# Optimization experiments

Measured on AMD Instinct MI355X. Metric: run time of the kernel, lower is better.

Reference implementation:

```python
import jax, jax.numpy as jnp
import numpy as np

B = 16        # graphs per batch
N0 = 4096     # nodes per graph (equal-size graphs -> static TopK shapes)
DEG = 8       # avg degree
E = B * N0 * DEG
CW = 64
OUT = 256


def _seg_sum(vals, idx, n):
    return jax.ops.segment_sum(vals, idx, num_segments=n)


def _sage(x, src, dst, valid, wl, bl, wr, n):
    # PyG SAGEConv: lin_l(mean_{j->i} x_j) + lin_r(x_i); lin_r has no bias
    vf = valid.astype(x.dtype)
    msg = x[src] * vf[:, None]                     # [E, d]
    s = _seg_sum(msg, dst, n)
    cnt = _seg_sum(vf, dst, n)
    mean = s / jnp.maximum(cnt, 1.0)[:, None]
    return mean @ wl.T + bl + x @ wr.T


def _gcn(x, src, dst, valid, w, b, n):
    # PyG GCNConv: add self-loops, symmetric normalization
    h = x @ w.T
    vf = valid.astype(x.dtype)
    deg = 1.0 + _seg_sum(vf, dst, n)               # includes self-loop
    inv_sqrt = jax.lax.rsqrt(deg)
    norm = inv_sqrt[src] * inv_sqrt[dst] * vf      # [E]
    agg = _seg_sum(h[src] * norm[:, None], dst, n) + h * (1.0 / deg)[:, None]
    return agg + b


def _topk_pool(x, src, dst, valid, w, n_per_graph):
    # PyG TopKPooling: score = x@w/||w||, keep top ceil(ratio*n) per graph,
    # x' = x[perm] * tanh(score[perm]); reindex edges, drop edges with removed endpoints.
    k = (n_per_graph + 1) // 2
    score = (x @ w) / jnp.linalg.norm(w)
    vals, idx = jax.lax.top_k(score.reshape(B, n_per_graph), k)   # [B,k]
    offs = (jnp.arange(B, dtype=jnp.int32) * n_per_graph)[:, None]
    perm = (idx.astype(jnp.int32) + offs).reshape(-1)             # [B*k] global ids
    x_new = x[perm] * jnp.tanh(vals.reshape(-1))[:, None]
    new_idx = jnp.full((B * n_per_graph,), -1, dtype=jnp.int32).at[perm].set(
        jnp.arange(B * k, dtype=jnp.int32))
    s2, d2 = new_idx[src], new_idx[dst]
    valid2 = valid & (s2 >= 0) & (d2 >= 0)
    s2 = jnp.where(valid2, s2, 0)
    d2 = jnp.where(valid2, d2, 0)
    return x_new, s2, d2, valid2, k


def _readout(x, k):
    xg = x.reshape(B, k, -1)
    return jnp.concatenate([xg.max(axis=1), xg.mean(axis=1)], axis=1)  # [B, 2d]


def _forward(x, edge_src, edge_dst, w1_l, b1, w1_r, w2_l, b2, w2_r, w3_l, b3, w3_r,
             w4, b4, w5, b5, w6, b6, p1, p2, p3, p4, p5, p6,
             lw1, lb1, lw2, lb2, lw3, lb3):
    src, dst = edge_src, edge_dst
    valid = jnp.ones((E,), dtype=bool)
    n = N0
    sage_ps = [(w1_l, b1, w1_r), (w2_l, b2, w2_r), (w3_l, b3, w3_r)]
    gcn_ps = [(w4, b4), (w5, b5), (w6, b6)]
    pools = [p1, p2, p3, p4, p5, p6]
    h = x
    z = None
    for i in range(6):
        if i < 3:
            wl, bl, wr = sage_ps[i]
            h = jax.nn.relu(_sage(h, src, dst, valid, wl, bl, wr, B * n))
        else:
            w, b = gcn_ps[i - 3]
            h = jax.nn.relu(_gcn(h, src, dst, valid, w, b, B * n))
        h, src, dst, valid, n = _topk_pool(h, src, dst, valid, pools[i], n)
        r = _readout(h, n)
        z = r if z is None else z + r
    z = jax.nn.relu(z @ lw1.T + lb1)
    z = jax.nn.relu(z @ lw2.T + lb2)
    z = z @ lw3.T + lb3
    return jax.nn.softmax(z, axis=1)


def setup_inputs() -> dict:
    key = jax.random.key(0)
    ks = jax.random.split(key, 40)

    def nrm(k, shape, s=0.1):
        return jax.random.normal(k, shape, dtype=jnp.float32) * s

    # per-graph random edges (both endpoints inside the same graph block)
    epg = N0 * DEG
    src_l = jax.random.randint(ks[0], (B, epg), 0, N0, dtype=jnp.int32)
    dst_l = jax.random.randint(ks[1], (B, epg), 0, N0, dtype=jnp.int32)
    offs = (jnp.arange(B, dtype=jnp.int32) * N0)[:, None]
    inp = {
        'x': jax.random.normal(ks[2], (B * N0, 2), dtype=jnp.float32),
        'edge_src': (src_l + offs).reshape(-1),
        'edge_dst': (dst_l + offs).reshape(-1),
        'w1_l': nrm(ks[3], (CW, 2)), 'b1': nrm(ks[4], (CW,)), 'w1_r': nrm(ks[5], (CW, 2)),
        'w2_l': nrm(ks[6], (CW, CW)), 'b2': nrm(ks[7], (CW,)), 'w2_r': nrm(ks[8], (CW, CW)),
        'w3_l': nrm(ks[9], (CW, CW)), 'b3': nrm(ks[10], (CW,)), 'w3_r': nrm(ks[11], (CW, CW)),
        'w4': nrm(ks[12], (CW, CW)), 'b4': jnp.zeros((CW,), jnp.float32),
        'w5': nrm(ks[13], (CW, CW)), 'b5': jnp.zeros((CW,), jnp.float32),
        'w6': nrm(ks[14], (CW, CW)), 'b6': jnp.zeros((CW,), jnp.float32),
        'p1': nrm(ks[15], (CW,)), 'p2': nrm(ks[16], (CW,)), 'p3': nrm(ks[17], (CW,)),
        'p4': nrm(ks[18], (CW,)), 'p5': nrm(ks[19], (CW,)), 'p6': nrm(ks[20], (CW,)),
        'lw1': nrm(ks[21], (128, 2 * CW)), 'lb1': nrm(ks[22], (128,)),
        'lw2': nrm(ks[23], (64, 128)), 'lb2': nrm(ks[24], (64,)),
        'lw3': nrm(ks[25], (OUT, 64)), 'lb3': nrm(ks[26], (OUT,)),
    }
    return inp


def reference(x, edge_src, edge_dst, w1_l, b1, w1_r, w2_l, b2, w2_r, w3_l, b3, w3_r,
              w4, b4, w5, b5, w6, b6, p1, p2, p3, p4, p5, p6,
              lw1, lb1, lw2, lb2, lw3, lb3):
    return _forward(x, edge_src, edge_dst, w1_l, b1, w1_r, w2_l, b2, w2_r,
                    w3_l, b3, w3_r, w4, b4, w5, b5, w6, b6,
                    p1, p2, p3, p4, p5, p6, lw1, lb1, lw2, lb2, lw3, lb3)
```

## Files before the change

kernel.cpp:

```cpp
#include <hip/hip_runtime.h>
#include <math.h>

#define NB 16
#define N0 4096
#define NE 524288


static __global__ void k_count(const int* __restrict__ dst, int* __restrict__ cnt) {
  int e = blockIdx.x * 256 + threadIdx.x;
  if (e >= NE) return;
  atomicAdd(&cnt[dst[e]], 1);
}

static __global__ void k_fill0(const int* __restrict__ src, const int* __restrict__ dst,
                               int* __restrict__ cursor, int* __restrict__ list) {
  int e = blockIdx.x * 256 + threadIdx.x;
  if (e >= NE) return;
  int d = dst[e];
  int slot = atomicAdd(&cursor[d], 1);
  list[slot] = src[e];
}


static __global__ void k_scan1(const int* __restrict__ in, int* __restrict__ out,
                               int* __restrict__ bsum, int n) {
  __shared__ int ts[256];
  int base = blockIdx.x * 1024 + threadIdx.x * 4;
  int a0 = (base + 0 < n) ? in[base + 0] : 0;
  int a1 = (base + 1 < n) ? in[base + 1] : 0;
  int a2 = (base + 2 < n) ? in[base + 2] : 0;
  int a3 = (base + 3 < n) ? in[base + 3] : 0;
  int s = a0 + a1 + a2 + a3;
  ts[threadIdx.x] = s;
  __syncthreads();
  for (int off = 1; off < 256; off <<= 1) {
    int v = (threadIdx.x >= off) ? ts[threadIdx.x - off] : 0;
    __syncthreads();
    ts[threadIdx.x] += v;
    __syncthreads();
  }
  int excl = ts[threadIdx.x] - s;
  if (base + 0 < n) out[base + 0] = excl;
  excl += a0;
  if (base + 1 < n) out[base + 1] = excl;
  excl += a1;
  if (base + 2 < n) out[base + 2] = excl;
  excl += a2;
  if (base + 3 < n) out[base + 3] = excl;
  if (threadIdx.x == 255) bsum[blockIdx.x] = ts[255];
}

static __global__ void k_scan2(int* __restrict__ bsum, int nb) {
  __shared__ int t[64];
  int i = threadIdx.x;
  int v = (i < nb) ? bsum[i] : 0;
  t[i] = v;
  __syncthreads();
  for (int off = 1; off < 64; off <<= 1) {
    int u = (i >= off) ? t[i - off] : 0;
    __syncthreads();
    t[i] += u;
    __syncthreads();
  }
  if (i < nb) bsum[i] = t[i] - v;
}

static __global__ void k_scan3(int* __restrict__ out, const int* __restrict__ bsum, int n) {
  int i = blockIdx.x * 256 + threadIdx.x;
  if (i < n) out[i] += bsum[i >> 10];
}


static __global__ void k_newcount(const int* __restrict__ perm, const int* __restrict__ offs,
                                  const int* __restrict__ cnt, const int* __restrict__ list,
                                  const int* __restrict__ newidx, int* __restrict__ ncnt,
                                  int newn) {
  int nn = blockIdx.x * 256 + threadIdx.x;
  if (nn >= newn) return;
  int old = perm[nn];
  int st = offs[old], c = cnt[old];
  int cc = 0;
  for (int j = 0; j < c; ++j) cc += (newidx[list[st + j]] >= 0);
  ncnt[nn] = cc;
}

static __global__ void k_newfill(const int* __restrict__ perm, const int* __restrict__ offs,
                                 const int* __restrict__ cnt, const int* __restrict__ list,
                                 const int* __restrict__ newidx, const int* __restrict__ noffs,
                                 int* __restrict__ nlist, int newn) {
  int nn = blockIdx.x * 256 + threadIdx.x;
  if (nn >= newn) return;
  int old = perm[nn];
  int st = offs[old], c = cnt[old];
  int pos = noffs[nn];
  for (int j = 0; j < c; ++j) {
    int s2 = newidx[list[st + j]];
    if (s2 >= 0) nlist[pos++] = s2;
  }
}


static __global__ void k_pnorm(const float* __restrict__ p0, const float* __restrict__ p1,
                               const float* __restrict__ p2, const float* __restrict__ p3,
                               const float* __restrict__ p4, const float* __restrict__ p5,
                               float* __restrict__ pnbuf) {
  const float* pp = p0;
  switch (blockIdx.x) {
    case 1: pp = p1; break;
    case 2: pp = p2; break;
    case 3: pp = p3; break;
    case 4: pp = p4; break;
    case 5: pp = p5; break;
    default: break;
  }
  double v = (double)pp[threadIdx.x];
  v *= v;
#pragma unroll
  for (int off = 1; off < 64; off <<= 1) v += __shfl_xor(v, off);
  if (threadIdx.x == 0) pnbuf[blockIdx.x] = (float)(1.0 / sqrt(v));
}


static __global__ void k_sage_gather2(const float* __restrict__ x, const int* __restrict__ offs,
                                      const int* __restrict__ cnt, const int* __restrict__ list,
                                      float* __restrict__ mean, int ntot) {
  int v = blockIdx.x * 256 + threadIdx.x;
  if (v >= ntot) return;
  int st = offs[v], c = cnt[v];
  float s0 = 0.f, s1 = 0.f;
  for (int j = 0; j < c; ++j) {
    int s = list[st + j];
    s0 += x[s * 2 + 0];
    s1 += x[s * 2 + 1];
  }
  float inv = 1.0f / fmaxf((float)c, 1.0f);
  mean[v * 2 + 0] = s0 * inv;
  mean[v * 2 + 1] = s1 * inv;
}

static __global__ void k_sage_gather64(const float* __restrict__ x, const int* __restrict__ offs,
                                       const int* __restrict__ cnt, const int* __restrict__ list,
                                       float* __restrict__ mean, int ntot) {
  int lane = threadIdx.x & 63, vl = threadIdx.x >> 6;
  int v = blockIdx.x * 4 + vl;
  if (v >= ntot) return;
  int st = offs[v], c = cnt[v];
  float acc = 0.f;
  for (int j = 0; j < c; ++j) {
    int s = list[st + j];
    acc += x[(size_t)s * 64 + lane];
  }
  mean[(size_t)v * 64 + lane] = acc * (1.0f / fmaxf((float)c, 1.0f));
}

static __global__ void k_sage0(const float* __restrict__ x, const float* __restrict__ mean,
                               const float* __restrict__ wl, const float* __restrict__ blv,
                               const float* __restrict__ wr, const float* __restrict__ pvec,
                               const float* __restrict__ pnbuf, float* __restrict__ h,
                               float* __restrict__ score, int ntot) {
  __shared__ float wlT[2][65], wrT[2][65];
  if (threadIdx.x < 128) {
    int o = threadIdx.x >> 1, d = threadIdx.x & 1;
    wlT[d][o] = wl[o * 2 + d];
    wrT[d][o] = wr[o * 2 + d];
  }
  __syncthreads();
  int o = threadIdx.x & 63, vl = threadIdx.x >> 6;
  int base = blockIdx.x * 16 + vl * 4;
  float pn = pnbuf[0];
  float psl = pvec[o];
#pragma unroll
  for (int r = 0; r < 4; ++r) {
    int v = base + r;
    if (v >= ntot) break;
    float acc = blv[o] + mean[v * 2 + 0] * wlT[0][o] + mean[v * 2 + 1] * wlT[1][o] +
                x[v * 2 + 0] * wrT[0][o] + x[v * 2 + 1] * wrT[1][o];
    float hval = fmaxf(acc, 0.0f);
    h[(size_t)v * 64 + o] = hval;
    double sc = (double)hval * (double)psl;
#pragma unroll
    for (int off = 1; off < 64; off <<= 1) sc += __shfl_xor(sc, off);
    if (o == 0) score[v] = (float)sc * pn;
  }
}

static __global__ __launch_bounds__(256) void k_sage_mm(
    const float* __restrict__ x, const float* __restrict__ mean, const float* __restrict__ wl,
    const float* __restrict__ blv, const float* __restrict__ wr, const float* __restrict__ pvec,
    const float* __restrict__ pnbuf, int pidx, float* __restrict__ h,
    float* __restrict__ score) {
  __shared__ float smem[16384];
  __shared__ float psh[64], bsh[64];
  float* xT = smem;
  float* mT = smem + 4096;
  float* wlT = smem + 8192;
  float* wrT = smem + 12288;
  int t = threadIdx.x;
  size_t nb = blockIdx.x;

  const float4* wl4 = (const float4*)wl;
  const float4* wr4 = (const float4*)wr;
  for (int i4 = t; i4 < 1024; i4 += 256) {
    int o = i4 >> 4, db = (i4 & 15) << 2;
    float4 L = wl4[i4], R = wr4[i4];
    float Lv[4] = {L.x, L.y, L.z, L.w}, Rv[4] = {R.x, R.y, R.z, R.w};
    int og = o >> 2, o3 = o & 3;
#pragma unroll
    for (int j = 0; j < 4; ++j) {
      int d = db + j;
      int col = ((og ^ (d & 15)) << 2) | o3;
      wlT[(d << 6) + col] = Lv[j];
      wrT[(d << 6) + col] = Rv[j];
    }
  }
  if (t < 64) {
    psh[t] = pvec[t];
    bsh[t] = blv[t];
  }
  const float4* x4 = (const float4*)(x + nb * 4096);
  const float4* m4 = (const float4*)(mean + nb * 4096);
  for (int i = t; i < 1024; i += 256) {
    int node = i >> 4, db = (i & 15) << 2;
    float4 a = x4[i], m = m4[i];
    float av[4] = {a.x, a.y, a.z, a.w}, mv[4] = {m.x, m.y, m.z, m.w};
    int ng = node >> 2, n0 = node & 3;
#pragma unroll
    for (int j = 0; j < 4; ++j) {
      int d = db + j;
      int col = ((ng ^ (d & 15)) << 2) | n0;
      xT[(d << 6) + col] = av[j];
      mT[(d << 6) + col] = mv[j];
    }
  }
  __syncthreads();

  int tx = t & 15, ty = t >> 4;
  float acc[4][4] = {};
#pragma unroll 4
  for (int k = 0; k < 64; ++k) {
    int s = k & 15;
    int ca = (tx ^ s) << 2, cb = (ty ^ s) << 2;
    const float4 a = *(const float4*)&xT[(k << 6) + ca];
    const float4 m = *(const float4*)&mT[(k << 6) + ca];
    const float4 L = *(const float4*)&wlT[(k << 6) + cb];
    const float4 R = *(const float4*)&wrT[(k << 6) + cb];
    float A[4] = {a.x, a.y, a.z, a.w}, M[4] = {m.x, m.y, m.z, m.w};
    float Lv[4] = {L.x, L.y, L.z, L.w}, Rv[4] = {R.x, R.y, R.z, R.w};
#pragma unroll
    for (int r = 0; r < 4; ++r)
#pragma unroll
      for (int c = 0; c < 4; ++c) acc[r][c] += M[r] * Lv[c] + A[r] * Rv[c];
  }

  float pn = pnbuf[pidx];
  float hv[4][4];
  double sp[4];
#pragma unroll
  for (int r = 0; r < 4; ++r) {
    sp[r] = 0.0;
#pragma unroll
    for (int c = 0; c < 4; ++c) {
      float v = fmaxf(acc[r][c] + bsh[(ty << 2) + c], 0.0f);
      hv[r][c] = v;
      sp[r] += (double)v * (double)psh[(ty << 2) + c];
    }
  }
  __syncthreads();
  float* hT = smem;
  double* sred = (double*)(smem + 8192);
#pragma unroll
  for (int r = 0; r < 4; ++r) {
    int node = (tx << 2) + r;
    int nk = node & 15;
#pragma unroll
    for (int c = 0; c < 4; ++c) hT[node * 68 + (((ty ^ nk) << 2) | c)] = hv[r][c];
    sred[(ty << 6) + node] = sp[r];
  }
  __syncthreads();
  float4* h4 = (float4*)(h + nb * 4096);
  for (int i = t; i < 1024; i += 256) {
    int node = i >> 4, q = i & 15;
    h4[i] = *(const float4*)&hT[node * 68 + ((q ^ (node & 15)) << 2)];
  }
  if (t < 64) {
    double ssum = 0.0;
    for (int g = 0; g < 16; ++g) ssum += sred[(g << 6) + t];
    score[nb * 64 + t] = (float)ssum * pn;
  }
}

static __global__ __launch_bounds__(256) void k_gcn_mm(const float* __restrict__ x,
                                                       const float* __restrict__ w,
                                                       float* __restrict__ h1) {
  __shared__ float smem[8192];
  float* xT = smem;
  float* wT = smem + 4096;
  int t = threadIdx.x;
  size_t nb = blockIdx.x;
  const float4* w4 = (const float4*)w;
  for (int i4 = t; i4 < 1024; i4 += 256) {
    int o = i4 >> 4, db = (i4 & 15) << 2;
    float4 W = w4[i4];
    float Wv[4] = {W.x, W.y, W.z, W.w};
    int og = o >> 2, o3 = o & 3;
#pragma unroll
    for (int j = 0; j < 4; ++j) {
      int d = db + j;
      wT[(d << 6) + (((og ^ (d & 15)) << 2) | o3)] = Wv[j];
    }
  }
  const float4* x4 = (const float4*)(x + nb * 4096);
  for (int i = t; i < 1024; i += 256) {
    int node = i >> 4, db = (i & 15) << 2;
    float4 a = x4[i];
    float av[4] = {a.x, a.y, a.z, a.w};
    int ng = node >> 2, n0 = node & 3;
#pragma unroll
    for (int j = 0; j < 4; ++j) {
      int d = db + j;
      xT[(d << 6) + (((ng ^ (d & 15)) << 2) | n0)] = av[j];
    }
  }
  __syncthreads();
  int tx = t & 15, ty = t >> 4;
  float acc[4][4] = {};
#pragma unroll 4
  for (int k = 0; k < 64; ++k) {
    int s = k & 15;
    const float4 a = *(const float4*)&xT[(k << 6) + ((tx ^ s) << 2)];
    const float4 W = *(const float4*)&wT[(k << 6) + ((ty ^ s) << 2)];
    float A[4] = {a.x, a.y, a.z, a.w}, Wv[4] = {W.x, W.y, W.z, W.w};
#pragma unroll
    for (int r = 0; r < 4; ++r)
#pragma unroll
      for (int c = 0; c < 4; ++c) acc[r][c] += A[r] * Wv[c];
  }
  __syncthreads();
  float* hT = smem;
#pragma unroll
  for (int r = 0; r < 4; ++r) {
    int node = (tx << 2) + r;
    int nk = node & 15;
#pragma unroll
    for (int c = 0; c < 4; ++c) hT[node * 68 + (((ty ^ nk) << 2) | c)] = acc[r][c];
  }
  __syncthreads();
  float4* h4 = (float4*)(h1 + nb * 4096);
  for (int i = t; i < 1024; i += 256) {
    int node = i >> 4, q = i & 15;
    h4[i] = *(const float4*)&hT[node * 68 + ((q ^ (node & 15)) << 2)];
  }
}

static __global__ void k_gcn_gather(const float* __restrict__ h1, const int* __restrict__ offs,
                                    const int* __restrict__ cnt, const int* __restrict__ list,
                                    const float* __restrict__ b, const float* __restrict__ pvec,
                                    const float* __restrict__ pnbuf, int pidx,
                                    float* __restrict__ h, float* __restrict__ score, int ntot) {
  int lane = threadIdx.x & 63, vl = threadIdx.x >> 6;
  int v = blockIdx.x * 4 + vl;
  if (v >= ntot) return;
  int st = offs[v], c = cnt[v];
  float degv = 1.0f + (float)c;
  float ivd = 1.0f / sqrtf(degv);
  float acc = 0.f;
  for (int j = 0; j < c; ++j) {
    int s = list[st + j];
    float nrm = (1.0f / sqrtf(1.0f + (float)cnt[s])) * ivd;
    acc += h1[(size_t)s * 64 + lane] * nrm;
  }
  float outv = fmaxf(acc + h1[(size_t)v * 64 + lane] * (1.0f / degv) + b[lane], 0.0f);
  h[(size_t)v * 64 + lane] = outv;
  double sc = (double)outv * (double)pvec[lane];
#pragma unroll
  for (int off = 1; off < 64; off <<= 1) sc += __shfl_xor(sc, off);
  if (lane == 0) score[v] = (float)sc * pnbuf[pidx];
}


static __global__ void k_chunksort(const float* __restrict__ score,
                                   unsigned long long* __restrict__ runs, int n_per, int k,
                                   int* __restrict__ newidx, int* __restrict__ perm, int single) {
  extern __shared__ unsigned long long sk[];
  int CH = blockDim.x;
  int g0 = blockIdx.x * CH;
  int b = g0 / n_per;
  int i = threadIdx.x;
  int gi = g0 + i;
  int li = gi - b * n_per;
  unsigned u = __float_as_uint(score[gi]);
  unsigned s = (u & 0x80000000u) ? u : ~(u | 0x80000000u);
  sk[i] = ((unsigned long long)s << 32) | (unsigned)li;
  __syncthreads();
  for (int ksz = 2; ksz <= CH; ksz <<= 1) {
    for (int j = ksz >> 1; j > 0; j >>= 1) {
      int ixj = i ^ j;
      if (ixj > i) {
        unsigned long long a = sk[i], c = sk[ixj];
        bool up = ((i & ksz) == 0);
        if ((a > c) == up) {
          sk[i] = c;
          sk[ixj] = a;
        }
      }
      __syncthreads();
    }
  }
  if (!single) {
    runs[gi] = sk[i];
  } else {
    int r = i;
    int idx = (int)(sk[r] & 0xFFFFFFFFu);
    int gidx = b * n_per + idx;
    if (r < k) {
      perm[b * k + r] = gidx;
      newidx[gidx] = b * k + r;
    } else {
      newidx[gidx] = -1;
    }
  }
}

static __global__ void k_merge(const unsigned long long* __restrict__ in,
                               unsigned long long* __restrict__ out, int L, int ntot, int n_per,
                               int k, int* __restrict__ newidx, int* __restrict__ perm,
                               int final) {
  int g = blockIdx.x * 256 + threadIdx.x;
  if (g >= ntot) return;
  unsigned long long key = in[g];
  int pair = g / (2 * L);
  int base = pair * 2 * L;
  int t = g - base;
  const unsigned long long* sib;
  int p;
  if (t < L) {
    sib = in + base + L;
    p = t;
  } else {
    sib = in + base;
    p = t - L;
  }
  int lo = 0, hi = L;
  while (lo < hi) {
    int mid = (lo + hi) >> 1;
    lo = (sib[mid] < key) ? mid + 1 : lo;
    hi = (sib[mid] < key) ? hi : mid;
  }
  int pos = p + lo;
  if (!final) {
    out[base + pos] = key;
  } else {
    int b = base / n_per;
    int idx = (int)(key & 0xFFFFFFFFu);
    int gidx = b * n_per + idx;
    if (pos < k) {
      perm[b * k + pos] = gidx;
      newidx[gidx] = b * k + pos;
    } else {
      newidx[gidx] = -1;
    }
  }
}

static __global__ void k_gather(const float* __restrict__ h, const float* __restrict__ score,
                                const int* __restrict__ perm, float* __restrict__ xnew, int kt) {
  int t = blockIdx.x * 256 + threadIdx.x;
  if (t >= kt * 16) return;
  int nn = t >> 4, q = t & 15;
  int old = perm[nn];
  float tm = tanhf(score[old]);
  float4 v = *(const float4*)&h[(size_t)old * 64 + q * 4];
  v.x *= tm; v.y *= tm; v.z *= tm; v.w *= tm;
  *(float4*)&xnew[(size_t)nn * 64 + q * 4] = v;
}


static __global__ void k_readout_part(const float* __restrict__ xnew, float* __restrict__ pmax,
                                      float* __restrict__ psum, int k, int nch) {
  int b = blockIdx.x / nch, c = blockIdx.x % nch;
  int d = threadIdx.x & 63, sl = threadIdx.x >> 6;
  int rpc = k / nch;
  const float* p = xnew + ((size_t)b * k + (size_t)c * rpc) * 64 + d;
  float m = -INFINITY, s = 0.0f;
  for (int r = sl; r < rpc; r += 4) {
    float v = p[(size_t)r * 64];
    m = fmaxf(m, v);
    s += v;
  }
  __shared__ float sm[4][64], ss[4][64];
  sm[sl][d] = m;
  ss[sl][d] = s;
  __syncthreads();
  if (sl == 0) {
    m = fmaxf(fmaxf(sm[0][d], sm[1][d]), fmaxf(sm[2][d], sm[3][d]));
    s = ss[0][d] + ss[1][d] + ss[2][d] + ss[3][d];
    pmax[(size_t)blockIdx.x * 64 + d] = m;
    psum[(size_t)blockIdx.x * 64 + d] = s;
  }
}

static __global__ void k_readout_comb(const float* __restrict__ pmax,
                                      const float* __restrict__ psum, float* __restrict__ z,
                                      int k, int nch) {
  int b = blockIdx.x, d = threadIdx.x;
  float m = -INFINITY, s = 0.0f;
  for (int c = 0; c < nch; ++c) {
    m = fmaxf(m, pmax[((size_t)b * nch + c) * 64 + d]);
    s += psum[((size_t)b * nch + c) * 64 + d];
  }
  z[b * 128 + d] += m;
  z[b * 128 + 64 + d] += s / (float)k;
}


static __global__ void k_mlp(const float* __restrict__ z, const float* __restrict__ lw1,
                             const float* __restrict__ lb1, const float* __restrict__ lw2,
                             const float* __restrict__ lb2, const float* __restrict__ lw3,
                             const float* __restrict__ lb3, float* __restrict__ out) {
  __shared__ float zs[128], t1[128], t2[64], t3[256], red[256];
  int b = blockIdx.x, tid = threadIdx.x;
  if (tid < 128) zs[tid] = z[b * 128 + tid];
  __syncthreads();
  if (tid < 128) {
    double a = 0.0;
    for (int d = 0; d < 128; ++d) a += (double)lw1[tid * 128 + d] * (double)zs[d];
    t1[tid] = fmaxf((float)a + lb1[tid], 0.0f);
  }
  __syncthreads();
  if (tid < 64) {
    double a = 0.0;
    for (int d = 0; d < 128; ++d) a += (double)lw2[tid * 128 + d] * (double)t1[d];
    t2[tid] = fmaxf((float)a + lb2[tid], 0.0f);
  }
  __syncthreads();
  {
    double a = 0.0;
    for (int d = 0; d < 64; ++d) a += (double)lw3[tid * 64 + d] * (double)t2[d];
    t3[tid] = (float)a + lb3[tid];
  }
  __syncthreads();
  red[tid] = t3[tid];
  __syncthreads();
  for (int s = 128; s > 0; s >>= 1) {
    if (tid < s) red[tid] = fmaxf(red[tid], red[tid + s]);
    __syncthreads();
  }
  float mx = red[0];
  __syncthreads();
  float e = expf(t3[tid] - mx);
  red[tid] = e;
  __syncthreads();
  for (int s = 128; s > 0; s >>= 1) {
    if (tid < s) red[tid] += red[tid + s];
    __syncthreads();
  }
  out[b * 256 + tid] = e / red[0];
}


extern "C" void kernel_launch(void* const* d_in, const int* in_sizes, int n_in,
                              void* d_out, int out_size, void* d_ws, size_t ws_size,
                              hipStream_t stream) {
  const float* x0 = (const float*)d_in[0];
  const int* esrc0 = (const int*)d_in[1];
  const int* edst0 = (const int*)d_in[2];
  const float* WL[3] = {(const float*)d_in[3], (const float*)d_in[6], (const float*)d_in[9]};
  const float* BL[3] = {(const float*)d_in[4], (const float*)d_in[7], (const float*)d_in[10]};
  const float* WR[3] = {(const float*)d_in[5], (const float*)d_in[8], (const float*)d_in[11]};
  const float* WG[3] = {(const float*)d_in[12], (const float*)d_in[14], (const float*)d_in[16]};
  const float* BG[3] = {(const float*)d_in[13], (const float*)d_in[15], (const float*)d_in[17]};
  const float* P[6] = {(const float*)d_in[18], (const float*)d_in[19], (const float*)d_in[20],
                       (const float*)d_in[21], (const float*)d_in[22], (const float*)d_in[23]};
  const float* lw1 = (const float*)d_in[24];
  const float* lb1 = (const float*)d_in[25];
  const float* lw2 = (const float*)d_in[26];
  const float* lb2 = (const float*)d_in[27];
  const float* lw3 = (const float*)d_in[28];
  const float* lb3 = (const float*)d_in[29];

  char* ws = (char*)d_ws;
  size_t off = 0;
  auto alloc = [&](size_t bytes) -> void* {
    void* p = ws + off;
    off += (bytes + 255) & ~(size_t)255;
    return p;
  };
  float* hA = (float*)alloc((size_t)65536 * 64 * 4);
  float* hB = (float*)alloc((size_t)32768 * 64 * 4);
  float* mean = (float*)alloc((size_t)32768 * 64 * 4);
  float* tmp = (float*)alloc((size_t)8192 * 64 * 4);
  float* score = (float*)alloc((size_t)65536 * 4);
  int* newidx = (int*)alloc((size_t)65536 * 4);
  int* perm = (int*)alloc((size_t)32768 * 4);
  int* cntA = (int*)alloc((size_t)65536 * 4);
  int* cntB = (int*)alloc((size_t)65536 * 4);
  int* offsA = (int*)alloc((size_t)65536 * 4);
  int* offsB = (int*)alloc((size_t)65536 * 4);
  int* cursor = (int*)alloc((size_t)65536 * 4);
  int* bsum = (int*)alloc((size_t)64 * 4);
  int* listA = (int*)alloc((size_t)NE * 4);
  int* listB = (int*)alloc((size_t)NE * 4);
  float* z = (float*)alloc((size_t)16 * 128 * 4);
  float* pmax = (float*)alloc((size_t)NB * 32 * 64 * 4);
  float* psum = (float*)alloc((size_t)NB * 32 * 64 * 4);
  unsigned long long* keyA = (unsigned long long*)alloc((size_t)65536 * 8);
  unsigned long long* keyB = (unsigned long long*)alloc((size_t)65536 * 8);
  float* pnbuf = (float*)alloc((size_t)64 * 4);
  if (off > ws_size) return;

  auto scan = [&](int* cntp, int* offsp, int n) {
    int nblk = (n + 1023) / 1024;
    k_scan1<<<nblk, 256, 0, stream>>>(cntp, offsp, bsum, n);
    k_scan2<<<1, 64, 0, stream>>>(bsum, nblk);
    k_scan3<<<(n + 255) / 256, 256, 0, stream>>>(offsp, bsum, n);
  };

  hipMemsetAsync(z, 0, 16 * 128 * 4, stream);
  k_pnorm<<<6, 64, 0, stream>>>(P[0], P[1], P[2], P[3], P[4], P[5], pnbuf);

  hipMemsetAsync(cntA, 0, (size_t)65536 * 4, stream);
  k_count<<<NE / 256, 256, 0, stream>>>(edst0, cntA);
  scan(cntA, offsA, 65536);
  hipMemcpyAsync(cursor, offsA, (size_t)65536 * 4, hipMemcpyDeviceToDevice, stream);
  k_fill0<<<NE / 256, 256, 0, stream>>>(esrc0, edst0, cursor, listA);

  const float* xcur = x0;
  int* ccnt = cntA;
  int* coffs = offsA;
  int* clist = listA;

  for (int i = 0; i < 6; ++i) {
    int n_per = N0 >> i;
    int ntot = NB * n_per;
    int k = n_per >> 1;

    if (i == 0) {
      k_sage_gather2<<<(ntot + 255) / 256, 256, 0, stream>>>(xcur, coffs, ccnt, clist, mean, ntot);
      k_sage0<<<(ntot + 15) / 16, 256, 0, stream>>>(xcur, mean, WL[0], BL[0], WR[0], P[0], pnbuf,
                                                    hA, score, ntot);
    } else if (i < 3) {
      k_sage_gather64<<<(ntot + 3) / 4, 256, 0, stream>>>(xcur, coffs, ccnt, clist, mean, ntot);
      k_sage_mm<<<ntot / 64, 256, 0, stream>>>(xcur, mean, WL[i], BL[i], WR[i], P[i], pnbuf, i,
                                               hA, score);
    } else {
      int g = i - 3;
      k_gcn_mm<<<ntot / 64, 256, 0, stream>>>(xcur, WG[g], tmp);
      k_gcn_gather<<<(ntot + 3) / 4, 256, 0, stream>>>(tmp, coffs, ccnt, clist, BG[g], P[i],
                                                       pnbuf, i, hA, score, ntot);
    }

    int CH = (n_per < 256) ? n_per : 256;
    int single = (CH == n_per) ? 1 : 0;
    k_chunksort<<<ntot / CH, CH, (size_t)CH * 8, stream>>>(score, keyA, n_per, k, newidx, perm,
                                                           single);
    if (!single) {
      unsigned long long* cur = keyA;
      unsigned long long* nxt = keyB;
      for (int L = CH; L * 2 <= n_per; L <<= 1) {
        int fin = (L * 2 == n_per) ? 1 : 0;
        k_merge<<<(ntot + 255) / 256, 256, 0, stream>>>(cur, nxt, L, ntot, n_per, k, newidx, perm,
                                                        fin);
        unsigned long long* t = cur;
        cur = nxt;
        nxt = t;
      }
    }
    k_gather<<<(NB * k * 16 + 255) / 256, 256, 0, stream>>>(hA, score, perm, hB, NB * k);

    if (i < 5) {
      int newn = NB * k;
      int* ncnt = (i & 1) ? cntA : cntB;
      int* noffs = (i & 1) ? offsA : offsB;
      int* nlist = (i & 1) ? listA : listB;
      k_newcount<<<(newn + 255) / 256, 256, 0, stream>>>(perm, coffs, ccnt, clist, newidx, ncnt,
                                                         newn);
      scan(ncnt, noffs, newn);
      k_newfill<<<(newn + 255) / 256, 256, 0, stream>>>(perm, coffs, ccnt, clist, newidx, noffs,
                                                        nlist, newn);
      ccnt = ncnt;
      coffs = noffs;
      clist = nlist;
    }

    int nch = (k >= 64) ? (k / 64) : 1;
    k_readout_part<<<NB * nch, 256, 0, stream>>>(hB, pmax, psum, k, nch);
    k_readout_comb<<<NB, 64, 0, stream>>>(pmax, psum, z, k, nch);
    xcur = hB;
  }

  k_mlp<<<NB, 256, 0, stream>>>(z, lw1, lb1, lw2, lb2, lw3, lb3, (float*)d_out);
}
```

Baseline: 418.8 us.

## Fuse scan, SAGE gather, and pooled gather with readout; enlarge sort chunk

Replaces the three-kernel prefix scan (plus a device copy) with a single 1024-thread block scan that can also write the cursor copy. Folds the 64-wide neighbour-mean gather into the SAGE matmul kernel so the mean goes straight to shared memory without a global round trip. Fuses the TopK feature gather with the per-chunk max/sum readout, and raises the chunk-sort size from 256 to 1024 to cut merge passes. Risks include a serial single-block scan, per-thread loops over 16 nodes raising register pressure, and the readout assuming k is a multiple of 64.

```diff
diff --git a/kernel.cpp b/kernel.cpp
--- a/kernel.cpp
+++ b/kernel.cpp
@@ -22,52 +22,37 @@
 }
 
 
-static __global__ void k_scan1(const int* __restrict__ in, int* __restrict__ out,
-                               int* __restrict__ bsum, int n) {
-  __shared__ int ts[256];
-  int base = blockIdx.x * 1024 + threadIdx.x * 4;
-  int a0 = (base + 0 < n) ? in[base + 0] : 0;
-  int a1 = (base + 1 < n) ? in[base + 1] : 0;
-  int a2 = (base + 2 < n) ? in[base + 2] : 0;
-  int a3 = (base + 3 < n) ? in[base + 3] : 0;
-  int s = a0 + a1 + a2 + a3;
-  ts[threadIdx.x] = s;
-  __syncthreads();
-  for (int off = 1; off < 256; off <<= 1) {
-    int v = (threadIdx.x >= off) ? ts[threadIdx.x - off] : 0;
+static __global__ __launch_bounds__(1024) void k_scan_one(const int* __restrict__ in,
+                                                          int* __restrict__ out,
+                                                          int* __restrict__ out2, int n) {
+  __shared__ int ts[1024];
+  int t = threadIdx.x;
+  int E = n >> 10;
+  int base = t * E;
+  int loc = 0;
+#pragma unroll 4
+  for (int j = 0; j < E; ++j) loc += in[base + j];
+  ts[t] = loc;
+  __syncthreads();
+  for (int off = 1; off < 1024; off <<= 1) {
+    int v = (t >= off) ? ts[t - off] : 0;
     __syncthreads();
-    ts[threadIdx.x] += v;
+    ts[t] += v;
     __syncthreads();
   }
-  int excl = ts[threadIdx.x] - s;
-  if (base + 0 < n) out[base + 0] = excl;
-  excl += a0;
-  if (base + 1 < n) out[base + 1] = excl;
-  excl += a1;
-  if (base + 2 < n) out[base + 2] = excl;
-  excl += a2;
-  if (base + 3 < n) out[base + 3] = excl;
-  if (threadIdx.x == 255) bsum[blockIdx.x] = ts[255];
-}
-
-static __global__ void k_scan2(int* __restrict__ bsum, int nb) {
-  __shared__ int t[64];
-  int i = threadIdx.x;
-  int v = (i < nb) ? bsum[i] : 0;
-  t[i] = v;
-  __syncthreads();
-  for (int off = 1; off < 64; off <<= 1) {
-    int u = (i >= off) ? t[i - off] : 0;
-    __syncthreads();
-    t[i] += u;
-    __syncthreads();
-  }
-  if (i < nb) bsum[i] = t[i] - v;
-}
-
-static __global__ void k_scan3(int* __restrict__ out, const int* __restrict__ bsum, int n) {
-  int i = blockIdx.x * 256 + threadIdx.x;
-  if (i < n) out[i] += bsum[i >> 10];
+  int run = ts[t] - loc;
+  if (out2) {
+    for (int j = 0; j < E; ++j) {
+      out[base + j] = run;
+      out2[base + j] = run;
+      run += in[base + j];
+    }
+  } else {
+    for (int j = 0; j < E; ++j) {
+      out[base + j] = run;
+      run += in[base + j];
+    }
+  }
 }
 
 
@@ -138,21 +123,6 @@
   mean[v * 2 + 1] = s1 * inv;
 }
 
-static __global__ void k_sage_gather64(const float* __restrict__ x, const int* __restrict__ offs,
-                                       const int* __restrict__ cnt, const int* __restrict__ list,
-                                       float* __restrict__ mean, int ntot) {
-  int lane = threadIdx.x & 63, vl = threadIdx.x >> 6;
-  int v = blockIdx.x * 4 + vl;
-  if (v >= ntot) return;
-  int st = offs[v], c = cnt[v];
-  float acc = 0.f;
-  for (int j = 0; j < c; ++j) {
-    int s = list[st + j];
-    acc += x[(size_t)s * 64 + lane];
-  }
-  mean[(size_t)v * 64 + lane] = acc * (1.0f / fmaxf((float)c, 1.0f));
-}
-
 static __global__ void k_sage0(const float* __restrict__ x, const float* __restrict__ mean,
                                const float* __restrict__ wl, const float* __restrict__ blv,
                                const float* __restrict__ wr, const float* __restrict__ pvec,
@@ -185,8 +155,9 @@
 }
 
 static __global__ __launch_bounds__(256) void k_sage_mm(
-    const float* __restrict__ x, const float* __restrict__ mean, const float* __restrict__ wl,
-    const float* __restrict__ blv, const float* __restrict__ wr, const float* __restrict__ pvec,
+    const float* __restrict__ x, const int* __restrict__ offs, const int* __restrict__ cnt,
+    const int* __restrict__ list, const float* __restrict__ wl, const float* __restrict__ blv,
+    const float* __restrict__ wr, const float* __restrict__ pvec,
     const float* __restrict__ pnbuf, int pidx, float* __restrict__ h,
     float* __restrict__ score) {
   __shared__ float smem[16384];
@@ -218,18 +189,42 @@
     bsh[t] = blv[t];
   }
   const float4* x4 = (const float4*)(x + nb * 4096);
-  const float4* m4 = (const float4*)(mean + nb * 4096);
   for (int i = t; i < 1024; i += 256) {
     int node = i >> 4, db = (i & 15) << 2;
-    float4 a = x4[i], m = m4[i];
-    float av[4] = {a.x, a.y, a.z, a.w}, mv[4] = {m.x, m.y, m.z, m.w};
+    float4 a = x4[i];
+    float av[4] = {a.x, a.y, a.z, a.w};
     int ng = node >> 2, n0 = node & 3;
 #pragma unroll
     for (int j = 0; j < 4; ++j) {
       int d = db + j;
-      int col = ((ng ^ (d & 15)) << 2) | n0;
-      xT[(d << 6) + col] = av[j];
-      mT[(d << 6) + col] = mv[j];
+      xT[(d << 6) + (((ng ^ (d & 15)) << 2) | n0)] = av[j];
+    }
+  }
+  {
+    int lane = t & 63, w = t >> 6;
+    int stq[16], cq[16];
+    float accq[16];
+    int cmax = 0;
+#pragma unroll
+    for (int q = 0; q < 16; ++q) {
+      int gv = (int)nb * 64 + w * 16 + q;
+      stq[q] = offs[gv];
+      cq[q] = cnt[gv];
+      accq[q] = 0.f;
+      cmax = max(cmax, cq[q]);
+    }
+    for (int j = 0; j < cmax; ++j) {
+#pragma unroll
+      for (int q = 0; q < 16; ++q) {
+        if (j < cq[q]) accq[q] += x[(size_t)list[stq[q] + j] * 64 + lane];
+      }
+    }
+#pragma unroll
+    for (int q = 0; q < 16; ++q) {
+      int node = w * 16 + q;
+      float mval = accq[q] * (1.0f / fmaxf((float)cq[q], 1.0f));
+      int col = (((node >> 2) ^ (lane & 15)) << 2) | (node & 3);
+      mT[(lane << 6) + col] = mval;
     }
   }
   __syncthreads();
@@ -288,6 +283,7 @@
     score[nb * 64 + t] = (float)ssum * pn;
   }
 }
+
 
 static __global__ __launch_bounds__(256) void k_gcn_mm(const float* __restrict__ x,
                                                        const float* __restrict__ w,
@@ -462,40 +458,47 @@
   }
 }
 
-static __global__ void k_gather(const float* __restrict__ h, const float* __restrict__ score,
-                                const int* __restrict__ perm, float* __restrict__ xnew, int kt) {
-  int t = blockIdx.x * 256 + threadIdx.x;
-  if (t >= kt * 16) return;
-  int nn = t >> 4, q = t & 15;
+
+static __global__ __launch_bounds__(1024) void k_gather_ro(
+    const float* __restrict__ h, const float* __restrict__ score, const int* __restrict__ perm,
+    float* __restrict__ xnew, float* __restrict__ pmax, float* __restrict__ psum) {
+  __shared__ float tile[64 * 68];
+  __shared__ float pm[16][65], ps[16][65];
+  int t = threadIdx.x;
+  int node = t >> 4, q = t & 15;
+  int nn = blockIdx.x * 64 + node;
   int old = perm[nn];
   float tm = tanhf(score[old]);
   float4 v = *(const float4*)&h[(size_t)old * 64 + q * 4];
-  v.x *= tm; v.y *= tm; v.z *= tm; v.w *= tm;
+  v.x *= tm;
+  v.y *= tm;
+  v.z *= tm;
+  v.w *= tm;
   *(float4*)&xnew[(size_t)nn * 64 + q * 4] = v;
-}
-
-
-static __global__ void k_readout_part(const float* __restrict__ xnew, float* __restrict__ pmax,
-                                      float* __restrict__ psum, int k, int nch) {
-  int b = blockIdx.x / nch, c = blockIdx.x % nch;
-  int d = threadIdx.x & 63, sl = threadIdx.x >> 6;
-  int rpc = k / nch;
-  const float* p = xnew + ((size_t)b * k + (size_t)c * rpc) * 64 + d;
-  float m = -INFINITY, s = 0.0f;
-  for (int r = sl; r < rpc; r += 4) {
-    float v = p[(size_t)r * 64];
-    m = fmaxf(m, v);
-    s += v;
-  }
-  __shared__ float sm[4][64], ss[4][64];
-  sm[sl][d] = m;
-  ss[sl][d] = s;
-  __syncthreads();
-  if (sl == 0) {
-    m = fmaxf(fmaxf(sm[0][d], sm[1][d]), fmaxf(sm[2][d], sm[3][d]));
-    s = ss[0][d] + ss[1][d] + ss[2][d] + ss[3][d];
-    pmax[(size_t)blockIdx.x * 64 + d] = m;
-    psum[(size_t)blockIdx.x * 64 + d] = s;
+  *(float4*)&tile[node * 68 + ((q ^ (node & 15)) << 2)] = v;
+  __syncthreads();
+  int slot = t >> 6, d = t & 63;
+  int q2 = d >> 2, i3 = d & 3;
+  float m = -INFINITY, s = 0.f;
+#pragma unroll
+  for (int r = 0; r < 4; ++r) {
+    int nd = slot * 4 + r;
+    float val = tile[nd * 68 + (((q2 ^ (nd & 15)) << 2) | i3)];
+    m = fmaxf(m, val);
+    s += val;
+  }
+  pm[slot][d] = m;
+  ps[slot][d] = s;
+  __syncthreads();
+  if (t < 64) {
+    float mm = -INFINITY, ss = 0.f;
+#pragma unroll
+    for (int sl = 0; sl < 16; ++sl) {
+      mm = fmaxf(mm, pm[sl][t]);
+      ss += ps[sl][t];
+    }
+    pmax[(size_t)blockIdx.x * 64 + t] = mm;
+    psum[(size_t)blockIdx.x * 64 + t] = ss;
   }
 }
 
@@ -587,7 +590,7 @@
   };
   float* hA = (float*)alloc((size_t)65536 * 64 * 4);
   float* hB = (float*)alloc((size_t)32768 * 64 * 4);
-  float* mean = (float*)alloc((size_t)32768 * 64 * 4);
+  float* mean = (float*)alloc((size_t)65536 * 2 * 4);
   float* tmp = (float*)alloc((size_t)8192 * 64 * 4);
   float* score = (float*)alloc((size_t)65536 * 4);
   int* newidx = (int*)alloc((size_t)65536 * 4);
@@ -597,7 +600,6 @@
   int* offsA = (int*)alloc((size_t)65536 * 4);
   int* offsB = (int*)alloc((size_t)65536 * 4);
   int* cursor = (int*)alloc((size_t)65536 * 4);
-  int* bsum = (int*)alloc((size_t)64 * 4);
   int* listA = (int*)alloc((size_t)NE * 4);
   int* listB = (int*)alloc((size_t)NE * 4);
   float* z = (float*)alloc((size_t)16 * 128 * 4);
@@ -608,20 +610,12 @@
   float* pnbuf = (float*)alloc((size_t)64 * 4);
   if (off > ws_size) return;
 
-  auto scan = [&](int* cntp, int* offsp, int n) {
-    int nblk = (n + 1023) / 1024;
-    k_scan1<<<nblk, 256, 0, stream>>>(cntp, offsp, bsum, n);
-    k_scan2<<<1, 64, 0, stream>>>(bsum, nblk);
-    k_scan3<<<(n + 255) / 256, 256, 0, stream>>>(offsp, bsum, n);
-  };
-
   hipMemsetAsync(z, 0, 16 * 128 * 4, stream);
   k_pnorm<<<6, 64, 0, stream>>>(P[0], P[1], P[2], P[3], P[4], P[5], pnbuf);
 
   hipMemsetAsync(cntA, 0, (size_t)65536 * 4, stream);
   k_count<<<NE / 256, 256, 0, stream>>>(edst0, cntA);
-  scan(cntA, offsA, 65536);
-  hipMemcpyAsync(cursor, offsA, (size_t)65536 * 4, hipMemcpyDeviceToDevice, stream);
+  k_scan_one<<<1, 1024, 0, stream>>>(cntA, offsA, cursor, 65536);
   k_fill0<<<NE / 256, 256, 0, stream>>>(esrc0, edst0, cursor, listA);
 
   const float* xcur = x0;
@@ -639,9 +633,8 @@
       k_sage0<<<(ntot + 15) / 16, 256, 0, stream>>>(xcur, mean, WL[0], BL[0], WR[0], P[0], pnbuf,
                                                     hA, score, ntot);
     } else if (i < 3) {
-      k_sage_gather64<<<(ntot + 3) / 4, 256, 0, stream>>>(xcur, coffs, ccnt, clist, mean, ntot);
-      k_sage_mm<<<ntot / 64, 256, 0, stream>>>(xcur, mean, WL[i], BL[i], WR[i], P[i], pnbuf, i,
-                                               hA, score);
+      k_sage_mm<<<ntot / 64, 256, 0, stream>>>(xcur, coffs, ccnt, clist, WL[i], BL[i], WR[i],
+                                               P[i], pnbuf, i, hA, score);
     } else {
       int g = i - 3;
       k_gcn_mm<<<ntot / 64, 256, 0, stream>>>(xcur, WG[g], tmp);
@@ -649,7 +642,7 @@
                                                        pnbuf, i, hA, score, ntot);
     }
 
-    int CH = (n_per < 256) ? n_per : 256;
+    int CH = (n_per < 1024) ? n_per : 1024;
     int single = (CH == n_per) ? 1 : 0;
     k_chunksort<<<ntot / CH, CH, (size_t)CH * 8, stream>>>(score, keyA, n_per, k, newidx, perm,
                                                            single);
@@ -660,12 +653,14 @@
         int fin = (L * 2 == n_per) ? 1 : 0;
         k_merge<<<(ntot + 255) / 256, 256, 0, stream>>>(cur, nxt, L, ntot, n_per, k, newidx, perm,
                                                         fin);
-        unsigned long long* t = cur;
+        unsigned long long* t2 = cur;
         cur = nxt;
-        nxt = t;
+        nxt = t2;
       }
     }
-    k_gather<<<(NB * k * 16 + 255) / 256, 256, 0, stream>>>(hA, score, perm, hB, NB * k);
+
+    int nch = k / 64;
+    k_gather_ro<<<NB * nch, 1024, 0, stream>>>(hA, score, perm, hB, pmax, psum);
 
     if (i < 5) {
       int newn = NB * k;
@@ -674,7 +669,7 @@
       int* nlist = (i & 1) ? listA : listB;
       k_newcount<<<(newn + 255) / 256, 256, 0, stream>>>(perm, coffs, ccnt, clist, newidx, ncnt,
                                                          newn);
-      scan(ncnt, noffs, newn);
+      k_scan_one<<<1, 1024, 0, stream>>>(ncnt, noffs, nullptr, newn);
       k_newfill<<<(newn + 255) / 256, 256, 0, stream>>>(perm, coffs, ccnt, clist, newidx, noffs,
                                                         nlist, newn);
       ccnt = ncnt;
@@ -682,8 +677,6 @@
       clist = nlist;
     }
 
-    int nch = (k >= 64) ? (k / 64) : 1;
-    k_readout_part<<<NB * nch, 256, 0, stream>>>(hB, pmax, psum, k, nch);
     k_readout_comb<<<NB, 64, 0, stream>>>(pmax, psum, z, k, nch);
     xcur = hB;
   }
```

Result: slower. 585.9 us (+39.9%).
